# Performance work log

Measured on AMD Instinct MI355X. Metric: run time of the kernel, lower is better.

Reference implementation:

```python
import jax, jax.numpy as jnp
import numpy as np

# ---- static config ----
B, H, W, C = 32, 64, 64, 256
WS, SHIFT, NH = 8, 4, 8
HD = C // NH
N = WS * WS  # tokens per window
NW = (H // WS) * (W // WS)
EPS = 1e-5


def _relative_position_index(ws):
    ch, cw = np.meshgrid(np.arange(ws), np.arange(ws), indexing='ij')
    coords = np.stack([ch, cw]).reshape(2, -1)          # (2, N)
    rel = coords[:, :, None] - coords[:, None, :]        # (2, N, N)
    rel = rel.transpose(1, 2, 0)
    rel[:, :, 0] += ws - 1
    rel[:, :, 1] += ws - 1
    rel[:, :, 0] *= 2 * ws - 1
    return jnp.asarray(rel.sum(-1))                      # (N, N) int


def _shifted_window_mask(h, w, ws, shift):
    img = np.zeros((h, w))
    slices = (slice(0, -ws), slice(-ws, -shift), slice(-shift, None))
    cnt = 0
    for hs in slices:
        for wsl in slices:
            img[hs, wsl] = cnt
            cnt += 1
    mw = img.reshape(h // ws, ws, w // ws, ws).transpose(0, 2, 1, 3).reshape(-1, ws * ws)
    diff = mw[:, None, :] - mw[:, :, None]
    return jnp.asarray(np.where(diff != 0, -100.0, 0.0).astype(np.float32))  # (nW, N, N)


REL_IDX = _relative_position_index(WS)
ATTN_MASK = _shifted_window_mask(H, W, WS, SHIFT)


def _layernorm(x, g, b):
    mu = jnp.mean(x, axis=-1, keepdims=True)
    var = jnp.mean(jnp.square(x - mu), axis=-1, keepdims=True)
    return (x - mu) * jax.lax.rsqrt(var + EPS) * g + b


def _window_partition(x):  # (B,H,W,C) -> (B*nW, N, C)
    x = x.reshape(B, H // WS, WS, W // WS, WS, C)
    return x.transpose(0, 1, 3, 2, 4, 5).reshape(-1, N, C)


def _window_reverse(win):  # (B*nW, N, C) -> (B,H,W,C)
    x = win.reshape(B, H // WS, W // WS, WS, WS, C)
    return x.transpose(0, 1, 3, 2, 4, 5).reshape(B, H, W, C)


def setup_inputs() -> dict:
    key = jax.random.key(0)
    ks = jax.random.split(key, 6)
    s = lambda fan_in: 1.0 / np.sqrt(fan_in)
    return {
        'x': jax.random.normal(ks[0], (B, H * W, C), jnp.float32),
        'norm1_g': jnp.ones((C,), jnp.float32),
        'norm1_b': jnp.zeros((C,), jnp.float32),
        'qkv_w': jax.random.normal(ks[1], (C, 3 * C), jnp.float32) * s(C),
        'qkv_b': jnp.zeros((3 * C,), jnp.float32),
        'proj_w': jax.random.normal(ks[2], (C, C), jnp.float32) * s(C),
        'proj_b': jnp.zeros((C,), jnp.float32),
        'bias_table': jax.random.normal(ks[3], ((2 * WS - 1) ** 2, NH), jnp.float32) * 0.02,
        'norm2_g': jnp.ones((C,), jnp.float32),
        'norm2_b': jnp.zeros((C,), jnp.float32),
        'fc1_w': jax.random.normal(ks[4], (C, 4 * C), jnp.float32) * s(C),
        'fc1_b': jnp.zeros((4 * C,), jnp.float32),
        'fc2_w': jax.random.normal(ks[5], (4 * C, C), jnp.float32) * s(4 * C),
        'fc2_b': jnp.zeros((C,), jnp.float32),
    }


def reference(x, norm1_g, norm1_b, qkv_w, qkv_b, proj_w, proj_b, bias_table,
              norm2_g, norm2_b, fc1_w, fc1_b, fc2_w, fc2_b):
    shortcut = x
    h = _layernorm(x, norm1_g, norm1_b).reshape(B, H, W, C)
    # cyclic shift
    h = jnp.roll(h, shift=(-SHIFT, -SHIFT), axis=(1, 2))
    xw = _window_partition(h)                               # (Bw, N, C), Bw = B*nW
    # window attention
    qkv = xw @ qkv_w + qkv_b                                 # (Bw, N, 3C)
    qkv = qkv.reshape(-1, N, 3, NH, HD).transpose(2, 0, 3, 1, 4)
    q, k, v = qkv[0], qkv[1], qkv[2]                         # (Bw, NH, N, HD)
    attn = jnp.einsum('whnd,whmd->whnm', q * (HD ** -0.5), k)
    rpb = bias_table[REL_IDX.reshape(-1)].reshape(N, N, NH).transpose(2, 0, 1)
    attn = attn + rpb[None]
    attn = attn.reshape(B, NW, NH, N, N) + ATTN_MASK[None, :, None]
    attn = jax.nn.softmax(attn.reshape(-1, NH, N, N), axis=-1)
    out = jnp.einsum('whnm,whmd->whnd', attn, v)
    out = out.transpose(0, 2, 1, 3).reshape(-1, N, C)
    out = out @ proj_w + proj_b
    # reverse windows + shift back
    h = _window_reverse(out)
    h = jnp.roll(h, shift=(SHIFT, SHIFT), axis=(1, 2)).reshape(B, H * W, C)
    x = shortcut + h
    # MLP with pre-norm residual
    m = _layernorm(x, norm2_g, norm2_b)
    m = jax.nn.gelu(m @ fc1_w + fc1_b, approximate=False) @ fc2_w + fc2_b
    return x + m
```

## Files before the change

kernel.cpp:

```cpp
#include <hip/hip_runtime.h>
#include <hip/hip_bf16.h>


typedef __bf16 bf16;
typedef __bf16 bf16x8 __attribute__((ext_vector_type(8)));
typedef __bf16 bf16x4 __attribute__((ext_vector_type(4)));
typedef float  f32x4  __attribute__((ext_vector_type(4)));

#define GLDS(gp, lp)                                                                   \
    __builtin_amdgcn_global_load_lds(                                                  \
        (const __attribute__((address_space(1))) unsigned int*)(gp),                   \
        (__attribute__((address_space(3))) unsigned int*)(lp), 16, 0, 0)

__global__ __launch_bounds__(256) void prep_all(const float* __restrict__ qkv_w,
                                                const float* __restrict__ proj_w,
                                                const float* __restrict__ fc1_w,
                                                const float* __restrict__ fc2_w,
                                                const float* __restrict__ bt,
                                                bf16* __restrict__ WQ, bf16* __restrict__ WP,
                                                bf16* __restrict__ W1, bf16* __restrict__ W2,
                                                float* __restrict__ rpb) {
    int idx = blockIdx.x * 256 + threadIdx.x;
    if (idx < 196608) {
        int k = idx / 768, n = idx - k * 768;
        WQ[(size_t)n * 256 + k] = (bf16)qkv_w[idx];
    } else if (idx < 262144) {
        int l = idx - 196608;
        int k = l >> 8, n = l & 255;
        WP[(size_t)n * 256 + k] = (bf16)proj_w[l];
    } else if (idx < 524288) {
        int l = idx - 262144;
        int k = l >> 10, n = l & 1023;
        W1[(size_t)n * 256 + k] = (bf16)fc1_w[l];
    } else if (idx < 786432) {
        int l = idx - 524288;
        int k = l >> 8, n = l & 255;
        W2[(size_t)n * 1024 + k] = (bf16)fc2_w[l];
    } else {
        int l = idx - 786432;
        int h = l >> 12, n = (l >> 6) & 63, m = l & 63;
        int ridx = ((n >> 3) - (m >> 3) + 7) * 15 + ((n & 7) - (m & 7) + 7);
        rpb[l] = bt[ridx * 8 + h];
    }
}

__global__ __launch_bounds__(256) void ln_k(const float* __restrict__ x,
                                            const float* __restrict__ g,
                                            const float* __restrict__ bb,
                                            bf16* __restrict__ dst) {
    int t = blockIdx.x * 4 + (threadIdx.x >> 6);
    int lane = threadIdx.x & 63;
    int w = t >> 6, n = t & 63;
    int b = w >> 6, nw = w & 63;
    int r = ((nw >> 3) * 8 + (n >> 3) + 4) & 63;
    int c = ((nw & 7) * 8 + (n & 7) + 4) & 63;
    size_t src = ((size_t)b * 4096 + r * 64 + c) * 256;
    float4 v = *(const float4*)&x[src + lane * 4];
    float s = v.x + v.y + v.z + v.w;
    float sq = v.x * v.x + v.y * v.y + v.z * v.z + v.w * v.w;
#pragma unroll
    for (int off = 1; off < 64; off <<= 1) {
        s += __shfl_xor(s, off);
        sq += __shfl_xor(sq, off);
    }
    float mean = s * (1.0f / 256.0f);
    float var = sq * (1.0f / 256.0f) - mean * mean;
    float rstd = rsqrtf(var + 1e-5f);
    float4 gg = *(const float4*)&g[lane * 4];
    float4 bv = *(const float4*)&bb[lane * 4];
    bf16x4 o;
    o[0] = (bf16)((v.x - mean) * rstd * gg.x + bv.x);
    o[1] = (bf16)((v.y - mean) * rstd * gg.y + bv.y);
    o[2] = (bf16)((v.z - mean) * rstd * gg.z + bv.z);
    o[3] = (bf16)((v.w - mean) * rstd * gg.w + bv.w);
    *(bf16x4*)&dst[(size_t)t * 256 + lane * 4] = o;
}

__device__ __forceinline__ float fast_gelu(float v) {
    float t = v * v;
    float w = __builtin_fmaf(0.044715f * t, v, v);
    float e = __expf(-1.5957691216057308f * w);
    return v * __builtin_amdgcn_rcpf(1.0f + e);
}

template <int NDIM, int KDIM, int EPI>
__global__ __launch_bounds__(256) void gemm_k(const bf16* __restrict__ A,
                                              const bf16* __restrict__ Bt,
                                              const float* __restrict__ bias,
                                              bf16* __restrict__ outb,
                                              float* __restrict__ outf,
                                              const bf16* __restrict__ baseb) {
    __shared__ __align__(16) bf16 SH[24576];
    constexpr int NBN = NDIM / 128;
    constexpr int NK = KDIM / 32;
    const int tid = threadIdx.x;
    const int nwg = gridDim.x;
    const int flat = blockIdx.x;
    const int cpx = nwg >> 3;
    const int orig = (flat & 7) * cpx + (flat >> 3);
    const int bm = orig / NBN, bn = orig % NBN;

    const int lane = tid & 63, wid = tid >> 6;
    const int wr = wid >> 1, wc = wid & 1;
    const int lhi = lane >> 4, llo = lane & 15;

    f32x4 acc[4][4];
#pragma unroll
    for (int i = 0; i < 4; i++)
#pragma unroll
        for (int j = 0; j < 4; j++) acc[i][j] = f32x4{0.f, 0.f, 0.f, 0.f};

    const int srow = wid * 32 + (lane >> 2);
    const int scol = (((lane & 3) - ((lane >> 3) & 3)) & 3) * 8;
    const bf16* Ap = A + (size_t)(bm * 128 + srow) * KDIM + scol;
    const bf16* Bp = Bt + (size_t)(bn * 128 + srow) * KDIM + scol;
    const int gsw = ((lhi + (llo >> 1)) & 3) * 8;

#define STAGE(bufidx)                                                                  \
    do {                                                                               \
        bf16* Al = SH + (bufidx)*4096 + wid * 1024;                                    \
        bf16* Bl = SH + 12288 + (bufidx)*4096 + wid * 1024;                            \
        GLDS(Ap, Al);                                                                  \
        GLDS(Ap + 16 * KDIM, Al + 16 * 32);                                            \
        GLDS(Bp, Bl);                                                                  \
        GLDS(Bp + 16 * KDIM, Bl + 16 * 32);                                            \
        Ap += 32;                                                                      \
        Bp += 32;                                                                      \
    } while (0)

#define COMPUTE(bufidx)                                                                \
    do {                                                                               \
        const int ab = (bufidx)*4096;                                                  \
        bf16x8 af[4], bfr[4];                                                          \
        _Pragma("unroll") for (int mi = 0; mi < 4; mi++) af[mi] =                      \
            *(const bf16x8*)&SH[ab + (wr * 64 + mi * 16 + llo) * 32 + gsw];            \
        _Pragma("unroll") for (int ni = 0; ni < 4; ni++) bfr[ni] =                     \
            *(const bf16x8*)&SH[12288 + ab + (wc * 64 + ni * 16 + llo) * 32 + gsw];    \
        _Pragma("unroll") for (int mi = 0; mi < 4; mi++)                               \
            _Pragma("unroll") for (int ni = 0; ni < 4; ni++) acc[mi][ni] =             \
                __builtin_amdgcn_mfma_f32_16x16x32_bf16(bfr[ni], af[mi],               \
                                                        acc[mi][ni], 0, 0, 0);         \
    } while (0)

#define WAITBAR(N)                                                                     \
    asm volatile("s_waitcnt vmcnt(" #N ")" ::: "memory");                              \
    __builtin_amdgcn_s_barrier();                                                      \
    __builtin_amdgcn_sched_barrier(0)

#define END_PHASE                                                                      \
    asm volatile("s_waitcnt lgkmcnt(0)" ::: "memory");                                 \
    __builtin_amdgcn_s_barrier();                                                      \
    __builtin_amdgcn_sched_barrier(0)

    STAGE(0);
    STAGE(1);
    STAGE(2);
    int buf = 0;
    for (int i = 0; i + 3 < NK; ++i) {
        WAITBAR(8);
        COMPUTE(buf);
        END_PHASE;
        STAGE(buf);
        buf = (buf == 2) ? 0 : buf + 1;
    }
    WAITBAR(8);
    COMPUTE(buf);
    buf = (buf == 2) ? 0 : buf + 1;
    WAITBAR(4);
    COMPUTE(buf);
    buf = (buf == 2) ? 0 : buf + 1;
    WAITBAR(0);
    COMPUTE(buf);

#undef STAGE
#undef COMPUTE
#undef WAITBAR
#undef END_PHASE

    __syncthreads();

    char* shb = (char*)SH;
    if constexpr (EPI == 0 || EPI == 2) {
#pragma unroll
        for (int ni = 0; ni < 4; ni++) {
            const int lcol = wc * 64 + ni * 16 + lhi * 4;
            const float4 b4 = *(const float4*)&bias[bn * 128 + lcol];
#pragma unroll
            for (int mi = 0; mi < 4; mi++) {
                const int ltok = wr * 64 + mi * 16 + llo;
                float v0 = acc[mi][ni][0] + b4.x;
                float v1 = acc[mi][ni][1] + b4.y;
                float v2 = acc[mi][ni][2] + b4.z;
                float v3 = acc[mi][ni][3] + b4.w;
                bf16x4 o;
                if constexpr (EPI == 2) {
                    o[0] = (bf16)fast_gelu(v0); o[1] = (bf16)fast_gelu(v1);
                    o[2] = (bf16)fast_gelu(v2); o[3] = (bf16)fast_gelu(v3);
                } else {
                    o[0] = (bf16)v0; o[1] = (bf16)v1; o[2] = (bf16)v2; o[3] = (bf16)v3;
                }
                const int u2 = (lcol >> 3) ^ (ltok & 15);
                *(bf16x4*)(shb + ltok * 256 + u2 * 16 + (lcol & 7) * 2) = o;
            }
        }
        __syncthreads();
        const int j = lane & 15;
#pragma unroll
        for (int rnd = 0; rnd < 8; rnd++) {
            const int ltok = wid * 32 + rnd * 4 + (lane >> 4);
            const int u2 = j ^ (ltok & 15);
            bf16x8 v = *(const bf16x8*)(shb + ltok * 256 + u2 * 16);
            *(bf16x8*)&outb[(size_t)(bm * 128 + ltok) * NDIM + bn * 128 + j * 8] = v;
        }
    } else {
#pragma unroll
        for (int p = 0; p < 2; p++) {
            if (wc == p) {
#pragma unroll
                for (int ni = 0; ni < 4; ni++) {
                    const int lcolh = ni * 16 + lhi * 4;
                    const float4 b4 = *(const float4*)&bias[bn * 128 + p * 64 + lcolh];
#pragma unroll
                    for (int mi = 0; mi < 4; mi++) {
                        const int ltok = wr * 64 + mi * 16 + llo;
                        float4 o = {acc[mi][ni][0] + b4.x, acc[mi][ni][1] + b4.y,
                                    acc[mi][ni][2] + b4.z, acc[mi][ni][3] + b4.w};
                        const int u2 = (lcolh >> 2) ^ (ltok & 15);
                        *(float4*)(shb + ltok * 256 + u2 * 16) = o;
                    }
                }
            }
            __syncthreads();
            const int j = lane & 15;
#pragma unroll
            for (int rnd = 0; rnd < 8; rnd++) {
                const int ltok = wid * 32 + rnd * 4 + (lane >> 4);
                const int u2 = j ^ (ltok & 15);
                float4 v = *(const float4*)(shb + ltok * 256 + u2 * 16);
                const int gcol = bn * 128 + p * 64 + j * 4;
                const int grow = bm * 128 + ltok;
                size_t dst = (size_t)grow * NDIM + gcol;
                bf16x4 bb = *(const bf16x4*)&baseb[dst];
                float4 o = {v.x + (float)bb[0], v.y + (float)bb[1],
                            v.z + (float)bb[2], v.w + (float)bb[3]};
                *(float4*)&outf[dst] = o;
            }
            if (p == 0) __syncthreads();
        }
    }
}

__global__ __launch_bounds__(256) void proj_ln_k(const bf16* __restrict__ A,
                                                 const bf16* __restrict__ Bt,
                                                 const float* __restrict__ bias,
                                                 const float* __restrict__ resid,
                                                 bf16* __restrict__ baseb,
                                                 const float* __restrict__ g2,
                                                 const float* __restrict__ b2,
                                                 bf16* __restrict__ hb) {
    __shared__ __align__(16) bf16 SH[32768];
    constexpr int KDIM = 256;
    const int tid = threadIdx.x;
    const int nwg = gridDim.x;
    const int flat = blockIdx.x;
    const int cpx = nwg >> 3;
    const int bm = (flat & 7) * cpx + (flat >> 3);

    const int lane = tid & 63, wid = tid >> 6;
    const int lhi = lane >> 4, llo = lane & 15;

    f32x4 acc[4][4];
#pragma unroll
    for (int i = 0; i < 4; i++)
#pragma unroll
        for (int j = 0; j < 4; j++) acc[i][j] = f32x4{0.f, 0.f, 0.f, 0.f};

    const int scol = (((lane & 3) - ((lane >> 3) & 3)) & 3) * 8;
    const bf16* Ap = A + (size_t)(bm * 64 + wid * 16 + (lane >> 2)) * KDIM + scol;
    const bf16* Bp = Bt + (size_t)(wid * 64 + (lane >> 2)) * KDIM + scol;
    const int gsw = ((lhi + (llo >> 1)) & 3) * 8;

#define PSTAGE(bufidx)                                                                 \
    do {                                                                               \
        bf16* Al = SH + (bufidx)*2048 + wid * 512;                                     \
        bf16* Bl = SH + 6144 + (bufidx)*8192 + wid * 2048;                             \
        GLDS(Ap, Al);                                                                  \
        GLDS(Bp, Bl);                                                                  \
        GLDS(Bp + 16 * KDIM, Bl + 512);                                                \
        GLDS(Bp + 32 * KDIM, Bl + 1024);                                               \
        GLDS(Bp + 48 * KDIM, Bl + 1536);                                               \
        Ap += 32;                                                                      \
        Bp += 32;                                                                      \
    } while (0)

#define PCOMPUTE(bufidx)                                                               \
    do {                                                                               \
        bf16x8 af[4], bfr[4];                                                          \
        _Pragma("unroll") for (int mi = 0; mi < 4; mi++) af[mi] =                      \
            *(const bf16x8*)&SH[(bufidx)*2048 + (mi * 16 + llo) * 32 + gsw];           \
        _Pragma("unroll") for (int ni = 0; ni < 4; ni++) bfr[ni] =                     \
            *(const bf16x8*)&SH[6144 + (bufidx)*8192 +                                 \
                                (wid * 64 + ni * 16 + llo) * 32 + gsw];                \
        _Pragma("unroll") for (int mi = 0; mi < 4; mi++)                               \
            _Pragma("unroll") for (int ni = 0; ni < 4; ni++) acc[mi][ni] =             \
                __builtin_amdgcn_mfma_f32_16x16x32_bf16(bfr[ni], af[mi],               \
                                                        acc[mi][ni], 0, 0, 0);         \
    } while (0)

#define PWAITBAR(N)                                                                    \
    asm volatile("s_waitcnt vmcnt(" #N ")" ::: "memory");                              \
    __builtin_amdgcn_s_barrier();                                                      \
    __builtin_amdgcn_sched_barrier(0)

    PSTAGE(0);
    PSTAGE(1);
    PSTAGE(2);
    int buf = 0;
    for (int i = 0; i + 3 < 8; ++i) {
        PWAITBAR(10);
        PCOMPUTE(buf);
        asm volatile("s_waitcnt lgkmcnt(0)" ::: "memory");
        __builtin_amdgcn_s_barrier();
        __builtin_amdgcn_sched_barrier(0);
        PSTAGE(buf);
        buf = (buf == 2) ? 0 : buf + 1;
    }
    PWAITBAR(10);
    PCOMPUTE(buf);
    buf = (buf == 2) ? 0 : buf + 1;
    PWAITBAR(5);
    PCOMPUTE(buf);
    buf = (buf == 2) ? 0 : buf + 1;
    PWAITBAR(0);
    PCOMPUTE(buf);

#undef PSTAGE
#undef PCOMPUTE
#undef PWAITBAR

    __syncthreads();

    char* shb = (char*)SH;
#pragma unroll
    for (int ni = 0; ni < 4; ni++) {
        const int col0 = wid * 64 + ni * 16 + lhi * 4;
        const float4 b4 = *(const float4*)&bias[col0];
#pragma unroll
        for (int mi = 0; mi < 4; mi++) {
            const int ltok = mi * 16 + llo;
            float4 o = {acc[mi][ni][0] + b4.x, acc[mi][ni][1] + b4.y,
                        acc[mi][ni][2] + b4.z, acc[mi][ni][3] + b4.w};
            const int u2 = (col0 >> 2) ^ (ltok & 15);
            *(float4*)(shb + ltok * 1024 + u2 * 16) = o;
        }
    }
    __syncthreads();

    const float4 gg = *(const float4*)&g2[lane * 4];
    const float4 bb4 = *(const float4*)&b2[lane * 4];
#pragma unroll
    for (int rnd = 0; rnd < 16; rnd++) {
        const int t = rnd * 4 + wid;
        const int u2 = lane ^ (t & 15);
        float4 v = *(const float4*)(shb + t * 1024 + u2 * 16);
        const int grow = bm * 64 + t;
        int w = grow >> 6, n = grow & 63;
        int b = w >> 6, nw = w & 63;
        int rr = ((nw >> 3) * 8 + (n >> 3) + 4) & 63;
        int cc = ((nw & 7) * 8 + (n & 7) + 4) & 63;
        const size_t rowbase = ((size_t)b * 4096 + rr * 64 + cc) * 256;
        float4 rs = *(const float4*)&resid[rowbase + lane * 4];
        float4 o = {rs.x + v.x, rs.y + v.y, rs.z + v.z, rs.w + v.w};
        bf16x4 bo = {(bf16)o.x, (bf16)o.y, (bf16)o.z, (bf16)o.w};
        *(bf16x4*)&baseb[rowbase + lane * 4] = bo;
        float s = o.x + o.y + o.z + o.w;
        float sq = o.x * o.x + o.y * o.y + o.z * o.z + o.w * o.w;
#pragma unroll
        for (int off = 1; off < 64; off <<= 1) {
            s += __shfl_xor(s, off);
            sq += __shfl_xor(sq, off);
        }
        float mean = s * (1.0f / 256.0f);
        float var = sq * (1.0f / 256.0f) - mean * mean;
        float rstd = rsqrtf(var + 1e-5f);
        bf16x4 ho;
        ho[0] = (bf16)((o.x - mean) * rstd * gg.x + bb4.x);
        ho[1] = (bf16)((o.y - mean) * rstd * gg.y + bb4.y);
        ho[2] = (bf16)((o.z - mean) * rstd * gg.z + bb4.z);
        ho[3] = (bf16)((o.w - mean) * rstd * gg.w + bb4.w);
        *(bf16x4*)&hb[rowbase + lane * 4] = ho;
    }
}

__device__ __forceinline__ int regid3(int p) { return p < 56 ? 0 : (p < 60 ? 1 : 2); }

__global__ __launch_bounds__(256) void attn_k(const bf16* __restrict__ qkv,
                                              const float* __restrict__ rpb,
                                              bf16* __restrict__ aout) {
    __shared__ __align__(16) bf16 Pl[4][64 * 80];
    const int wid = threadIdx.x >> 6, lane = threadIdx.x & 63;
    const int lhi = lane >> 4, llo = lane & 15;
    const int wh = blockIdx.x * 4 + wid;
    const int w = wh >> 3, h = wh & 7;
    const bf16* base = qkv + (size_t)w * (64 * 768);

    bf16x8 qf[4], kf[4];
#pragma unroll
    for (int i = 0; i < 4; i++)
        qf[i] = *(const bf16x8*)(base + (i * 16 + llo) * 768 + h * 32 + lhi * 8);
#pragma unroll
    for (int i = 0; i < 4; i++)
        kf[i] = *(const bf16x8*)(base + (i * 16 + llo) * 768 + 256 + h * 32 + lhi * 8);
    f32x4 s[4][4];
#pragma unroll
    for (int mi = 0; mi < 4; mi++)
#pragma unroll
        for (int ni = 0; ni < 4; ni++) {
            s[mi][ni] = f32x4{0.f, 0.f, 0.f, 0.f};
            s[mi][ni] =
                __builtin_amdgcn_mfma_f32_16x16x32_bf16(qf[mi], kf[ni], s[mi][ni], 0, 0, 0);
        }

    const int nw = w & 63;
    const int pr0 = (nw >> 3) * 8, pc0 = (nw & 7) * 8;
    int creg[4];
#pragma unroll
    for (int ni = 0; ni < 4; ni++) {
        int m = ni * 16 + llo;
        creg[ni] = regid3(pr0 + (m >> 3)) * 3 + regid3(pc0 + (m & 7));
    }
    float rmax[4][4], rsum[4][4];
#pragma unroll
    for (int mi = 0; mi < 4; mi++)
#pragma unroll
        for (int r = 0; r < 4; r++) {
            int n = mi * 16 + lhi * 4 + r;
            int rreg = regid3(pr0 + (n >> 3)) * 3 + regid3(pc0 + (n & 7));
            float mx = -1e30f;
#pragma unroll
            for (int ni = 0; ni < 4; ni++) {
                int m = ni * 16 + llo;
                float sv = s[mi][ni][r] * 0.17677669529663687f + rpb[(h * 64 + n) * 64 + m] +
                           (rreg == creg[ni] ? 0.0f : -100.0f);
                s[mi][ni][r] = sv;
                mx = fmaxf(mx, sv);
            }
            rmax[mi][r] = mx;
        }
#pragma unroll
    for (int off = 1; off < 16; off <<= 1)
#pragma unroll
        for (int mi = 0; mi < 4; mi++)
#pragma unroll
            for (int r = 0; r < 4; r++)
                rmax[mi][r] = fmaxf(rmax[mi][r], __shfl_xor(rmax[mi][r], off));
#pragma unroll
    for (int mi = 0; mi < 4; mi++)
#pragma unroll
        for (int r = 0; r < 4; r++) {
            float a = 0.f;
#pragma unroll
            for (int ni = 0; ni < 4; ni++) {
                float p = __expf(s[mi][ni][r] - rmax[mi][r]);
                s[mi][ni][r] = p;
                a += p;
            }
            rsum[mi][r] = a;
        }
#pragma unroll
    for (int off = 1; off < 16; off <<= 1)
#pragma unroll
        for (int mi = 0; mi < 4; mi++)
#pragma unroll
            for (int r = 0; r < 4; r++) rsum[mi][r] += __shfl_xor(rsum[mi][r], off);

    bf16* P = Pl[wid];
#pragma unroll
    for (int mi = 0; mi < 4; mi++)
#pragma unroll
        for (int r = 0; r < 4; r++) {
            float rinv = 1.0f / rsum[mi][r];
            int row = mi * 16 + lhi * 4 + r;
#pragma unroll
            for (int ni = 0; ni < 4; ni++)
                P[row * 80 + ni * 16 + llo] = (bf16)(s[mi][ni][r] * rinv);
        }

    f32x4 o[4][2];
#pragma unroll
    for (int mi = 0; mi < 4; mi++)
#pragma unroll
        for (int ni = 0; ni < 2; ni++) o[mi][ni] = f32x4{0.f, 0.f, 0.f, 0.f};
#pragma unroll
    for (int kc = 0; kc < 2; kc++) {
        bf16x8 pf[4], vf[2];
#pragma unroll
        for (int mi = 0; mi < 4; mi++)
            pf[mi] = *(const bf16x8*)(P + (mi * 16 + llo) * 80 + kc * 32 + lhi * 8);
#pragma unroll
        for (int ni = 0; ni < 2; ni++)
#pragma unroll
            for (int j = 0; j < 8; j++)
                vf[ni][j] = base[(kc * 32 + lhi * 8 + j) * 768 + 512 + h * 32 + ni * 16 + llo];
#pragma unroll
        for (int mi = 0; mi < 4; mi++)
#pragma unroll
            for (int ni = 0; ni < 2; ni++)
                o[mi][ni] =
                    __builtin_amdgcn_mfma_f32_16x16x32_bf16(pf[mi], vf[ni], o[mi][ni], 0, 0, 0);
    }
#pragma unroll
    for (int mi = 0; mi < 4; mi++)
#pragma unroll
        for (int ni = 0; ni < 2; ni++)
#pragma unroll
            for (int r = 0; r < 4; r++) {
                int row = mi * 16 + lhi * 4 + r;
                aout[(size_t)(w * 64 + row) * 256 + h * 32 + ni * 16 + llo] =
                    (bf16)o[mi][ni][r];
            }
}

extern "C" void kernel_launch(void* const* d_in, const int* in_sizes, int n_in,
                              void* d_out, int out_size, void* d_ws, size_t ws_size,
                              hipStream_t stream) {
    const float* x      = (const float*)d_in[0];
    const float* n1g    = (const float*)d_in[1];
    const float* n1b    = (const float*)d_in[2];
    const float* qkv_w  = (const float*)d_in[3];
    const float* qkv_b  = (const float*)d_in[4];
    const float* proj_w = (const float*)d_in[5];
    const float* proj_b = (const float*)d_in[6];
    const float* btab   = (const float*)d_in[7];
    const float* n2g    = (const float*)d_in[8];
    const float* n2b    = (const float*)d_in[9];
    const float* fc1_w  = (const float*)d_in[10];
    const float* fc1_b  = (const float*)d_in[11];
    const float* fc2_w  = (const float*)d_in[12];
    const float* fc2_b  = (const float*)d_in[13];
    float* out = (float*)d_out;
    char* ws = (char*)d_ws;

    constexpr size_t MB = 1048576ull;
    bf16* XWc   = (bf16*)(ws);
    bf16* QKVc  = (bf16*)(ws + 17 * MB);
    bf16* ATTNc = (bf16*)(ws + 68 * MB);
    bf16* BASEc = (bf16*)(ws + 85 * MB);
    bf16* Hbc   = (bf16*)(ws + 102 * MB);
    bf16* Gc    = (bf16*)(ws + 119 * MB);
    bf16* WQ    = (bf16*)(ws + 187 * MB);
    bf16* WP    = (bf16*)(ws + 187 * MB + 393216);
    bf16* W1    = (bf16*)(ws + 187 * MB + 524288);
    bf16* W2    = (bf16*)(ws + 187 * MB + 1048576);
    float* RPB  = (float*)(ws + 187 * MB + 1572864);

    dim3 blk(256);
    prep_all<<<3200, blk, 0, stream>>>(qkv_w, proj_w, fc1_w, fc2_w, btab,
                                       WQ, WP, W1, W2, RPB);

    for (int c = 0; c < 4; ++c) {
        const size_t xo = (size_t)c * 32768 * 256;
        ln_k<<<8192, blk, 0, stream>>>(x + xo, n1g, n1b, XWc);
        gemm_k<768, 256, 0><<<1536, blk, 0, stream>>>(XWc, WQ, qkv_b, QKVc,
                                                      nullptr, nullptr);
        attn_k<<<1024, blk, 0, stream>>>(QKVc, RPB, ATTNc);
        proj_ln_k<<<512, blk, 0, stream>>>(ATTNc, WP, proj_b, x + xo, BASEc,
                                           n2g, n2b, Hbc);
        gemm_k<1024, 256, 2><<<2048, blk, 0, stream>>>(Hbc, W1, fc1_b, Gc,
                                                       nullptr, nullptr);
        gemm_k<256, 1024, 3><<<512, blk, 0, stream>>>(Gc, W2, fc2_b, nullptr,
                                                      out + xo, BASEc);
    }
}
```

Baseline: 532.7 us.

## Use 256x256 eight-wave GEMM tiles with quarter-phase pipelining and larger chunks

Replaces the 128x128, 4-wave GEMM with a 256x256 tile, 512-thread kernel that uses a double-buffered K=64 stage. Loads are split into four quarter stages interleaved with MFMA sub-phases, and MFMA issue priority is raised with setprio. Token chunking goes from 4 to 2 chunks, so each launch has more work, and the workspace buffers are reorganised (QKV and G alias). The aim is more operand reuse per LDS byte and fewer launches, at the cost of 128KB LDS per block, higher register pressure and fewer blocks for the fc2 GEMM.

```diff
diff --git a/kernel.cpp b/kernel.cpp
--- a/kernel.cpp
+++ b/kernel.cpp
@@ -84,15 +84,15 @@
 }
 
 template <int NDIM, int KDIM, int EPI>
-__global__ __launch_bounds__(256) void gemm_k(const bf16* __restrict__ A,
-                                              const bf16* __restrict__ Bt,
-                                              const float* __restrict__ bias,
-                                              bf16* __restrict__ outb,
-                                              float* __restrict__ outf,
-                                              const bf16* __restrict__ baseb) {
-    __shared__ __align__(16) bf16 SH[24576];
-    constexpr int NBN = NDIM / 128;
-    constexpr int NK = KDIM / 32;
+__global__ __launch_bounds__(512, 2) void gemm8_k(const bf16* __restrict__ A,
+                                                  const bf16* __restrict__ Bt,
+                                                  const float* __restrict__ bias,
+                                                  bf16* __restrict__ outb,
+                                                  float* __restrict__ outf,
+                                                  const bf16* __restrict__ baseb) {
+    __shared__ __align__(16) bf16 SH[65536];
+    constexpr int NBN = NDIM / 256;
+    constexpr int NT = KDIM / 64;
     const int tid = threadIdx.x;
     const int nwg = gridDim.x;
     const int flat = blockIdx.x;
@@ -101,93 +101,108 @@
     const int bm = orig / NBN, bn = orig % NBN;
 
     const int lane = tid & 63, wid = tid >> 6;
-    const int wr = wid >> 1, wc = wid & 1;
+    const int wm = wid >> 2, wn = wid & 3;
     const int lhi = lane >> 4, llo = lane & 15;
 
-    f32x4 acc[4][4];
-#pragma unroll
-    for (int i = 0; i < 4; i++)
+    f32x4 acc[8][4];
+#pragma unroll
+    for (int i = 0; i < 8; i++)
 #pragma unroll
         for (int j = 0; j < 4; j++) acc[i][j] = f32x4{0.f, 0.f, 0.f, 0.f};
 
-    const int srow = wid * 32 + (lane >> 2);
-    const int scol = (((lane & 3) - ((lane >> 3) & 3)) & 3) * 8;
-    const bf16* Ap = A + (size_t)(bm * 128 + srow) * KDIM + scol;
-    const bf16* Bp = Bt + (size_t)(bn * 128 + srow) * KDIM + scol;
-    const int gsw = ((lhi + (llo >> 1)) & 3) * 8;
-
-#define STAGE(bufidx)                                                                  \
+    const int srow = tid >> 3;
+    const int slg = ((tid & 7) - ((tid >> 3) & 7)) & 7;
+    const bf16* pA = A + (size_t)(bm * 256 + srow) * KDIM + slg * 8;
+    const bf16* pB = Bt + (size_t)(bn * 256 + srow) * KDIM + slg * 8;
+
+#define SU(ptr, base, h, i, buf, kt)                                                   \
+    GLDS(ptr + (size_t)((h)*128 + (i)*64) * KDIM + (kt)*64,                            \
+         SH + (base) + (buf)*16384 + (h)*8192 + (i)*4096 + tid * 8)
+#define STAGE_U(u, buf, kt)                                                            \
     do {                                                                               \
-        bf16* Al = SH + (bufidx)*4096 + wid * 1024;                                    \
-        bf16* Bl = SH + 12288 + (bufidx)*4096 + wid * 1024;                            \
-        GLDS(Ap, Al);                                                                  \
-        GLDS(Ap + 16 * KDIM, Al + 16 * 32);                                            \
-        GLDS(Bp, Bl);                                                                  \
-        GLDS(Bp + 16 * KDIM, Bl + 16 * 32);                                            \
-        Ap += 32;                                                                      \
-        Bp += 32;                                                                      \
+        if ((u) == 0) { SU(pA, 0, 0, 0, buf, kt); SU(pA, 0, 0, 1, buf, kt); }          \
+        else if ((u) == 1) { SU(pA, 0, 1, 0, buf, kt); SU(pA, 0, 1, 1, buf, kt); }     \
+        else if ((u) == 2) { SU(pB, 32768, 0, 0, buf, kt); SU(pB, 32768, 0, 1, buf, kt); } \
+        else { SU(pB, 32768, 1, 0, buf, kt); SU(pB, 32768, 1, 1, buf, kt); }           \
     } while (0)
 
-#define COMPUTE(bufidx)                                                                \
+    const int pg0 = (lhi + (llo & 7)) & 7;
+    const int rdA = (wm * 128 + llo) * 64;
+    const int rdB = 32768 + (wn * 64 + llo) * 64;
+
+    bf16x8 bq[4];
+
+#define QPHASE(buf, mh, ks, LOADB)                                                     \
     do {                                                                               \
-        const int ab = (bufidx)*4096;                                                  \
-        bf16x8 af[4], bfr[4];                                                          \
-        _Pragma("unroll") for (int mi = 0; mi < 4; mi++) af[mi] =                      \
-            *(const bf16x8*)&SH[ab + (wr * 64 + mi * 16 + llo) * 32 + gsw];            \
-        _Pragma("unroll") for (int ni = 0; ni < 4; ni++) bfr[ni] =                     \
-            *(const bf16x8*)&SH[12288 + ab + (wc * 64 + ni * 16 + llo) * 32 + gsw];    \
-        _Pragma("unroll") for (int mi = 0; mi < 4; mi++)                               \
-            _Pragma("unroll") for (int ni = 0; ni < 4; ni++) acc[mi][ni] =             \
-                __builtin_amdgcn_mfma_f32_16x16x32_bf16(bfr[ni], af[mi],               \
-                                                        acc[mi][ni], 0, 0, 0);         \
+        const int pg = (ks) ? (pg0 ^ 4) : pg0;                                         \
+        bf16x8 af0 = *(const bf16x8*)&SH[(buf)*16384 + rdA + ((mh)*4 + 0) * 1024 + pg * 8]; \
+        bf16x8 af1 = *(const bf16x8*)&SH[(buf)*16384 + rdA + ((mh)*4 + 1) * 1024 + pg * 8]; \
+        bf16x8 af2 = *(const bf16x8*)&SH[(buf)*16384 + rdA + ((mh)*4 + 2) * 1024 + pg * 8]; \
+        bf16x8 af3 = *(const bf16x8*)&SH[(buf)*16384 + rdA + ((mh)*4 + 3) * 1024 + pg * 8]; \
+        if (LOADB) {                                                                   \
+            _Pragma("unroll") for (int ni = 0; ni < 4; ni++) bq[ni] =                  \
+                *(const bf16x8*)&SH[(buf)*16384 + rdB + ni * 1024 + pg * 8];           \
+        }                                                                              \
+        asm volatile("s_waitcnt lgkmcnt(0)" ::: "memory");                             \
+        __builtin_amdgcn_sched_barrier(0);                                             \
+        __builtin_amdgcn_s_setprio(1);                                                 \
+        _Pragma("unroll") for (int ni = 0; ni < 4; ni++) {                             \
+            acc[(mh)*4 + 0][ni] = __builtin_amdgcn_mfma_f32_16x16x32_bf16(bq[ni], af0, acc[(mh)*4 + 0][ni], 0, 0, 0); \
+            acc[(mh)*4 + 1][ni] = __builtin_amdgcn_mfma_f32_16x16x32_bf16(bq[ni], af1, acc[(mh)*4 + 1][ni], 0, 0, 0); \
+            acc[(mh)*4 + 2][ni] = __builtin_amdgcn_mfma_f32_16x16x32_bf16(bq[ni], af2, acc[(mh)*4 + 2][ni], 0, 0, 0); \
+            acc[(mh)*4 + 3][ni] = __builtin_amdgcn_mfma_f32_16x16x32_bf16(bq[ni], af3, acc[(mh)*4 + 3][ni], 0, 0, 0); \
+        }                                                                              \
+        __builtin_amdgcn_s_setprio(0);                                                 \
     } while (0)
 
-#define WAITBAR(N)                                                                     \
-    asm volatile("s_waitcnt vmcnt(" #N ")" ::: "memory");                              \
+#define BAR                                                                            \
     __builtin_amdgcn_s_barrier();                                                      \
     __builtin_amdgcn_sched_barrier(0)
 
-#define END_PHASE                                                                      \
-    asm volatile("s_waitcnt lgkmcnt(0)" ::: "memory");                                 \
-    __builtin_amdgcn_s_barrier();                                                      \
-    __builtin_amdgcn_sched_barrier(0)
-
-    STAGE(0);
-    STAGE(1);
-    STAGE(2);
-    int buf = 0;
-    for (int i = 0; i + 3 < NK; ++i) {
-        WAITBAR(8);
-        COMPUTE(buf);
-        END_PHASE;
-        STAGE(buf);
-        buf = (buf == 2) ? 0 : buf + 1;
-    }
-    WAITBAR(8);
-    COMPUTE(buf);
-    buf = (buf == 2) ? 0 : buf + 1;
-    WAITBAR(4);
-    COMPUTE(buf);
-    buf = (buf == 2) ? 0 : buf + 1;
-    WAITBAR(0);
-    COMPUTE(buf);
-
-#undef STAGE
-#undef COMPUTE
-#undef WAITBAR
-#undef END_PHASE
+    STAGE_U(0, 0, 0);
+    STAGE_U(1, 0, 0);
+    STAGE_U(2, 0, 0);
+    STAGE_U(3, 0, 0);
+
+    for (int t = 0; t < NT; ++t) {
+        const int buf = t & 1, nb = buf ^ 1;
+        const bool pf = (t + 1 < NT);
+        if (pf) {
+            STAGE_U(0, nb, t + 1);
+            asm volatile("s_waitcnt vmcnt(2)" ::: "memory");
+        } else {
+            asm volatile("s_waitcnt vmcnt(0)" ::: "memory");
+        }
+        BAR;
+        QPHASE(buf, 0, 0, true);
+        BAR;
+        if (pf) STAGE_U(1, nb, t + 1);
+        QPHASE(buf, 1, 0, false);
+        BAR;
+        if (pf) STAGE_U(2, nb, t + 1);
+        QPHASE(buf, 0, 1, true);
+        BAR;
+        if (pf) STAGE_U(3, nb, t + 1);
+        QPHASE(buf, 1, 1, false);
+        BAR;
+    }
+
+#undef SU
+#undef STAGE_U
+#undef QPHASE
+#undef BAR
 
     __syncthreads();
-
     char* shb = (char*)SH;
+
     if constexpr (EPI == 0 || EPI == 2) {
 #pragma unroll
         for (int ni = 0; ni < 4; ni++) {
-            const int lcol = wc * 64 + ni * 16 + lhi * 4;
-            const float4 b4 = *(const float4*)&bias[bn * 128 + lcol];
-#pragma unroll
-            for (int mi = 0; mi < 4; mi++) {
-                const int ltok = wr * 64 + mi * 16 + llo;
+            const int col0 = wn * 64 + ni * 16 + lhi * 4;
+            const float4 b4 = *(const float4*)&bias[bn * 256 + col0];
+#pragma unroll
+            for (int mi = 0; mi < 8; mi++) {
+                const int row = wm * 128 + mi * 16 + llo;
                 float v0 = acc[mi][ni][0] + b4.x;
                 float v1 = acc[mi][ni][1] + b4.y;
                 float v2 = acc[mi][ni][2] + b4.z;
@@ -199,50 +214,50 @@
                 } else {
                     o[0] = (bf16)v0; o[1] = (bf16)v1; o[2] = (bf16)v2; o[3] = (bf16)v3;
                 }
-                const int u2 = (lcol >> 3) ^ (ltok & 15);
-                *(bf16x4*)(shb + ltok * 256 + u2 * 16 + (lcol & 7) * 2) = o;
+                const int byte = row * 512 + (((col0 >> 3) ^ (row & 31)) << 4) +
+                                 (col0 & 7) * 2;
+                *(bf16x4*)(shb + byte) = o;
             }
         }
         __syncthreads();
-        const int j = lane & 15;
-#pragma unroll
-        for (int rnd = 0; rnd < 8; rnd++) {
-            const int ltok = wid * 32 + rnd * 4 + (lane >> 4);
-            const int u2 = j ^ (ltok & 15);
-            bf16x8 v = *(const bf16x8*)(shb + ltok * 256 + u2 * 16);
-            *(bf16x8*)&outb[(size_t)(bm * 128 + ltok) * NDIM + bn * 128 + j * 8] = v;
+#pragma unroll
+        for (int it = 0; it < 16; it++) {
+            const int flat = it * 8192 + tid * 16;
+            const int row = flat >> 9;
+            const int g = tid & 31;
+            bf16x8 v = *(const bf16x8*)(shb + row * 512 + ((g ^ (row & 31)) << 4));
+            *(bf16x8*)&outb[(size_t)(bm * 256 + row) * NDIM + bn * 256 + g * 8] = v;
         }
     } else {
 #pragma unroll
         for (int p = 0; p < 2; p++) {
-            if (wc == p) {
+            if (wm == p) {
 #pragma unroll
                 for (int ni = 0; ni < 4; ni++) {
-                    const int lcolh = ni * 16 + lhi * 4;
-                    const float4 b4 = *(const float4*)&bias[bn * 128 + p * 64 + lcolh];
-#pragma unroll
-                    for (int mi = 0; mi < 4; mi++) {
-                        const int ltok = wr * 64 + mi * 16 + llo;
-                        float4 o = {acc[mi][ni][0] + b4.x, acc[mi][ni][1] + b4.y,
-                                    acc[mi][ni][2] + b4.z, acc[mi][ni][3] + b4.w};
-                        const int u2 = (lcolh >> 2) ^ (ltok & 15);
-                        *(float4*)(shb + ltok * 256 + u2 * 16) = o;
+                    const int gg = wn * 16 + ni * 4 + lhi;
+#pragma unroll
+                    for (int mi = 0; mi < 8; mi++) {
+                        const int row_l = mi * 16 + llo;
+                        float4 o = {acc[mi][ni][0], acc[mi][ni][1], acc[mi][ni][2],
+                                    acc[mi][ni][3]};
+                        *(float4*)(shb + row_l * 1024 + ((gg ^ (row_l & 31)) << 4)) = o;
                     }
                 }
             }
             __syncthreads();
-            const int j = lane & 15;
-#pragma unroll
-            for (int rnd = 0; rnd < 8; rnd++) {
-                const int ltok = wid * 32 + rnd * 4 + (lane >> 4);
-                const int u2 = j ^ (ltok & 15);
-                float4 v = *(const float4*)(shb + ltok * 256 + u2 * 16);
-                const int gcol = bn * 128 + p * 64 + j * 4;
-                const int grow = bm * 128 + ltok;
-                size_t dst = (size_t)grow * NDIM + gcol;
+#pragma unroll
+            for (int it = 0; it < 16; it++) {
+                const int flat = it * 8192 + tid * 16;
+                const int row_l = flat >> 10;
+                const int g = tid & 63;
+                float4 v = *(const float4*)(shb + row_l * 1024 + ((g ^ (row_l & 31)) << 4));
+                const int gcol = bn * 256 + g * 4;
+                const int grow = bm * 256 + p * 128 + row_l;
+                const float4 b4 = *(const float4*)&bias[gcol];
+                const size_t dst = (size_t)grow * NDIM + gcol;
                 bf16x4 bb = *(const bf16x4*)&baseb[dst];
-                float4 o = {v.x + (float)bb[0], v.y + (float)bb[1],
-                            v.z + (float)bb[2], v.w + (float)bb[3]};
+                float4 o = {v.x + b4.x + (float)bb[0], v.y + b4.y + (float)bb[1],
+                            v.z + b4.z + (float)bb[2], v.w + b4.w + (float)bb[3]};
                 *(float4*)&outf[dst] = o;
             }
             if (p == 0) __syncthreads();
@@ -543,32 +558,32 @@
 
     constexpr size_t MB = 1048576ull;
     bf16* XWc   = (bf16*)(ws);
-    bf16* QKVc  = (bf16*)(ws + 17 * MB);
-    bf16* ATTNc = (bf16*)(ws + 68 * MB);
-    bf16* BASEc = (bf16*)(ws + 85 * MB);
-    bf16* Hbc   = (bf16*)(ws + 102 * MB);
-    bf16* Gc    = (bf16*)(ws + 119 * MB);
-    bf16* WQ    = (bf16*)(ws + 187 * MB);
-    bf16* WP    = (bf16*)(ws + 187 * MB + 393216);
-    bf16* W1    = (bf16*)(ws + 187 * MB + 524288);
-    bf16* W2    = (bf16*)(ws + 187 * MB + 1048576);
-    float* RPB  = (float*)(ws + 187 * MB + 1572864);
-
-    dim3 blk(256);
-    prep_all<<<3200, blk, 0, stream>>>(qkv_w, proj_w, fc1_w, fc2_w, btab,
-                                       WQ, WP, W1, W2, RPB);
-
-    for (int c = 0; c < 4; ++c) {
-        const size_t xo = (size_t)c * 32768 * 256;
-        ln_k<<<8192, blk, 0, stream>>>(x + xo, n1g, n1b, XWc);
-        gemm_k<768, 256, 0><<<1536, blk, 0, stream>>>(XWc, WQ, qkv_b, QKVc,
-                                                      nullptr, nullptr);
-        attn_k<<<1024, blk, 0, stream>>>(QKVc, RPB, ATTNc);
-        proj_ln_k<<<512, blk, 0, stream>>>(ATTNc, WP, proj_b, x + xo, BASEc,
-                                           n2g, n2b, Hbc);
-        gemm_k<1024, 256, 2><<<2048, blk, 0, stream>>>(Hbc, W1, fc1_b, Gc,
+    bf16* QKVc  = (bf16*)(ws + 34 * MB);
+    bf16* Gc    = (bf16*)(ws + 34 * MB);
+    bf16* ATTNc = (bf16*)(ws + 169 * MB);
+    bf16* BASEc = (bf16*)(ws + 203 * MB);
+    bf16* Hbc   = (bf16*)(ws + 237 * MB);
+    bf16* WQ    = (bf16*)(ws + 272 * MB);
+    bf16* WP    = (bf16*)(ws + 272 * MB + 393216);
+    bf16* W1    = (bf16*)(ws + 272 * MB + 524288);
+    bf16* W2    = (bf16*)(ws + 272 * MB + 1048576);
+    float* RPB  = (float*)(ws + 272 * MB + 1572864);
+
+    dim3 b256(256), b512(512);
+    prep_all<<<3200, b256, 0, stream>>>(qkv_w, proj_w, fc1_w, fc2_w, btab,
+                                        WQ, WP, W1, W2, RPB);
+
+    for (int c = 0; c < 2; ++c) {
+        const size_t xo = (size_t)c * 65536 * 256;
+        ln_k<<<16384, b256, 0, stream>>>(x + xo, n1g, n1b, XWc);
+        gemm8_k<768, 256, 0><<<768, b512, 0, stream>>>(XWc, WQ, qkv_b, QKVc,
                                                        nullptr, nullptr);
-        gemm_k<256, 1024, 3><<<512, blk, 0, stream>>>(Gc, W2, fc2_b, nullptr,
-                                                      out + xo, BASEc);
-    }
-}
+        attn_k<<<2048, b256, 0, stream>>>(QKVc, RPB, ATTNc);
+        proj_ln_k<<<1024, b256, 0, stream>>>(ATTNc, WP, proj_b, x + xo, BASEc,
+                                             n2g, n2b, Hbc);
+        gemm8_k<1024, 256, 2><<<1024, b512, 0, stream>>>(Hbc, W1, fc1_b, Gc,
+                                                         nullptr, nullptr);
+        gemm8_k<256, 1024, 3><<<256, b512, 0, stream>>>(Gc, W2, fc2_b, nullptr,
+                                                        out + xo, BASEc);
+    }
+}
```

New measurement: 576.5 us. 1.08x slower.

## Restructure GEMM k-loop into single-barrier prefetch-before-compute pipeline

Applied to the files above, without the earlier changes.

The GEMM main loop changes from three stages in flight, with two barriers per k-step, to two stages in flight with one barrier per k-step. The next tile's global-to-LDS loads are now issued before the MFMA compute on the current buffer, so they overlap that compute. This removes one workgroup barrier and one waitcnt point per iteration. In exchange, each load has less lead time, since prefetch depth drops from three tiles to two, and memory latency may be less hidden.

```diff
diff --git a/kernel.cpp b/kernel.cpp
--- a/kernel.cpp
+++ b/kernel.cpp
@@ -142,40 +142,27 @@
                                                         acc[mi][ni], 0, 0, 0);         \
     } while (0)
 
-#define WAITBAR(N)                                                                     \
-    asm volatile("s_waitcnt vmcnt(" #N ")" ::: "memory");                              \
-    __builtin_amdgcn_s_barrier();                                                      \
-    __builtin_amdgcn_sched_barrier(0)
-
-#define END_PHASE                                                                      \
-    asm volatile("s_waitcnt lgkmcnt(0)" ::: "memory");                                 \
-    __builtin_amdgcn_s_barrier();                                                      \
-    __builtin_amdgcn_sched_barrier(0)
-
     STAGE(0);
     STAGE(1);
-    STAGE(2);
     int buf = 0;
-    for (int i = 0; i + 3 < NK; ++i) {
-        WAITBAR(8);
+    for (int i = 0; i < NK - 1; ++i) {
+        asm volatile("s_waitcnt vmcnt(4) lgkmcnt(0)" ::: "memory");
+        __builtin_amdgcn_s_barrier();
+        __builtin_amdgcn_sched_barrier(0);
+        if (i + 2 < NK) {
+            const int sb = (buf + 2 >= 3) ? buf - 1 : buf + 2;
+            STAGE(sb);
+        }
         COMPUTE(buf);
-        END_PHASE;
-        STAGE(buf);
         buf = (buf == 2) ? 0 : buf + 1;
     }
-    WAITBAR(8);
-    COMPUTE(buf);
-    buf = (buf == 2) ? 0 : buf + 1;
-    WAITBAR(4);
-    COMPUTE(buf);
-    buf = (buf == 2) ? 0 : buf + 1;
-    WAITBAR(0);
+    asm volatile("s_waitcnt vmcnt(0) lgkmcnt(0)" ::: "memory");
+    __builtin_amdgcn_s_barrier();
+    __builtin_amdgcn_sched_barrier(0);
     COMPUTE(buf);
 
 #undef STAGE
 #undef COMPUTE
-#undef WAITBAR
-#undef END_PHASE
 
     __syncthreads();
 
```

Measured after the change: 534.5 us. No clear change (+0.3%).
